# Performance work log

Hardware: AMD Instinct MI355X
Metric: run time of the kernel (lower is better)

Reference implementation:

```python
import jax, jax.numpy as jnp
import numpy as np

G, H, D = 8, 16, 64           # groups, heads-per-group, head_size
B, S = 2, 1024                # sequences, tokens per sequence (T = B*S packed)
HID = G * H * D               # 8192
SCALE = D ** -0.5


def _rotary(x, cos, sin):
    # NeoX-style rotary. x: [T, nh, D]; cos/sin: [T, D//2]
    half = D // 2
    c = cos[:, None, :]
    s = sin[:, None, :]
    x1, x2 = x[..., :half], x[..., half:]
    return jnp.concatenate([x1 * c - x2 * s, x2 * c + x1 * s], axis=-1)


def setup_inputs() -> dict:
    key = jax.random.key(0)
    ks = jax.random.split(key, 6)
    T = B * S
    hidden_states = jax.random.normal(ks[0], (T, HID), jnp.float32)
    # true rotary tables from positions (base 10000)
    pos = jnp.tile(jnp.arange(S, dtype=jnp.float32), B)            # [T]
    inv_freq = 1.0 / (10000.0 ** (jnp.arange(0, D, 2, dtype=jnp.float32) / D))
    freqs = pos[:, None] * inv_freq[None, :]                       # [T, D//2]
    cos, sin = jnp.cos(freqs), jnp.sin(freqs)
    w_qkv = jax.random.normal(ks[1], (HID, G * (H + 2) * D), jnp.float32) * (HID ** -0.5)
    b_qkv = jax.random.normal(ks[2], (G * (H + 2) * D,), jnp.float32) * 0.02
    w_dense = jax.random.normal(ks[3], (G * H * D, HID), jnp.float32) * (HID ** -0.5)
    b_dense = jax.random.normal(ks[4], (HID,), jnp.float32) * 0.02
    kv_cache = jnp.zeros((2, 4096, G, D), jnp.float32)
    slots = jnp.arange(T, dtype=jnp.int32)
    return dict(hidden_states=hidden_states, cos=cos, sin=sin,
                w_qkv=w_qkv, b_qkv=b_qkv, w_dense=w_dense, b_dense=b_dense,
                kv_cache=kv_cache, slots=slots, batch_size=B)


def reference(hidden_states, cos, sin, w_qkv, b_qkv, w_dense, b_dense,
              kv_cache, slots, batch_size):
    T = hidden_states.shape[0]
    qkv = hidden_states @ w_qkv + b_qkv                    # [T, G*(H+2)*D]
    qkv = qkv.reshape(T, G, H + 2, D)
    query = qkv[:, :, :H, :].reshape(T, G * H, D)          # [T, G*H, D]
    k = qkv[:, :, H, :]                                    # [T, G, D]
    v = qkv[:, :, H + 1, :]                                # [T, G, D]

    query = _rotary(query, cos, sin)
    k = _rotary(k, cos, sin)

    # reshape_and_cache: write rotated K and V into the slot cache
    new_cache = kv_cache.at[0, slots].set(k).at[1, slots].set(v)

    # prefill flash attention, causal, GQA (each group's K/V shared by H heads)
    q = query.reshape(batch_size, S, G, H, D)
    kb = k.reshape(batch_size, S, G, D)
    vb = v.reshape(batch_size, S, G, D)
    scores = jnp.einsum('bsghd,btgd->bghst', q, kb) * SCALE  # [B,G,H,S,S]
    causal = jnp.tril(jnp.ones((S, S), bool))
    scores = jnp.where(causal, scores, jnp.finfo(scores.dtype).min)
    probs = jax.nn.softmax(scores, axis=-1)
    attn = jnp.einsum('bghst,btgd->bsghd', probs, vb)        # [B,S,G,H,D]
    attn = attn.reshape(T, G * H * D)
    out = attn @ w_dense + b_dense                           # [T, HID]
    return out, new_cache
```

## Files before the change

kernel.cpp:

```cpp
#include <hip/hip_runtime.h>

#define T_TOK 2048
#define HIDD  8192
#define NQKV  9216
#define GG    8
#define HH    16
#define DD    64
#define SS    1024
#define BB    2
#define SCALE_ATTN 0.125f

typedef __attribute__((ext_vector_type(4))) float f32x4;
typedef __attribute__((ext_vector_type(8))) short bf16x8;

#define GLOBAL_AS __attribute__((address_space(1)))
#define LDS_AS    __attribute__((address_space(3)))

__device__ __forceinline__ void glds16(const void* g, void* l) {
  __builtin_amdgcn_global_load_lds((GLOBAL_AS void*)(g), (LDS_AS void*)(l), 16, 0, 0);
}

__device__ __forceinline__ ushort f2bf(float f) {
  union { float f; unsigned u; } v; v.f = f;
  unsigned u = v.u + 0x7fffu + ((v.u >> 16) & 1u);
  return (ushort)(u >> 16);
}

__global__ void cvt_bf16_kernel(const float* __restrict__ in, ushort* __restrict__ out, int n4) {
  int i = blockIdx.x * 256 + threadIdx.x;
  if (i >= n4) return;
  float4 v = ((const float4*)in)[i];
  ushort4 o;
  o.x = f2bf(v.x); o.y = f2bf(v.y); o.z = f2bf(v.z); o.w = f2bf(v.w);
  ((ushort4*)out)[i] = o;
}

__global__ void copy_f32_kernel(const float* __restrict__ in, float* __restrict__ out, int n4) {
  int i = blockIdx.x * 256 + threadIdx.x;
  if (i < n4) ((float4*)out)[i] = ((const float4*)in)[i];
}

__global__ __launch_bounds__(256) void transpose_bf16_kernel(
    const float* __restrict__ in, ushort* __restrict__ out, int R, int C)
{
  __shared__ float tile[64][65];
  const int c0 = blockIdx.x * 64, r0 = blockIdx.y * 64;
  const int tid = threadIdx.x;
  const int tx = tid & 15, iy = tid >> 4;
  #pragma unroll
  for (int p = 0; p < 4; ++p) {
    const int i = iy + p * 16;
    const float4 v = *(const float4*)&in[(size_t)(r0 + i) * C + c0 + tx * 4];
    tile[i][tx * 4 + 0] = v.x; tile[i][tx * 4 + 1] = v.y;
    tile[i][tx * 4 + 2] = v.z; tile[i][tx * 4 + 3] = v.w;
  }
  __syncthreads();
  const int r4 = tid & 15, cg = tid >> 4;
  #pragma unroll
  for (int p = 0; p < 4; ++p) {
    const int c = cg + p * 16;
    ushort4 o;
    o.x = f2bf(tile[r4 * 4 + 0][c]);
    o.y = f2bf(tile[r4 * 4 + 1][c]);
    o.z = f2bf(tile[r4 * 4 + 2][c]);
    o.w = f2bf(tile[r4 * 4 + 3][c]);
    *(ushort4*)&out[(size_t)(c0 + c) * R + r0 + r4 * 4] = o;
  }
}

__global__ __launch_bounds__(512, 2) void gemm_bt_kernel(
    const ushort* __restrict__ A, const ushort* __restrict__ Bt,
    const float* __restrict__ bias, float* __restrict__ C,
    int M, int N, int K)
{
  __shared__ __align__(16) ushort lds[4 * 16384];
  const int tid = threadIdx.x;
  const int wid = tid >> 6, lane = tid & 63;
  const int kg = lane >> 4, ln = lane & 15;

  const int nwg = gridDim.x * gridDim.y;
  const int lin = blockIdx.y * gridDim.x + blockIdx.x;
  const int swz = (lin & 7) * (nwg >> 3) + (lin >> 3);
  const int bx = swz % gridDim.x, by = swz / gridDim.x;

  const int m0 = by * 256, n0 = bx * 256;
  const int wm = (wid >> 2) << 7;
  const int wn = (wid & 3) << 6;

  f32x4 acc[8][4] = {};

  const int r0 = tid >> 2, sl = (tid & 3) * 8;
  const ushort* Ap0 = A  + (size_t)(m0 + r0) * K + sl;
  const ushort* Ap1 = A  + (size_t)(m0 + r0 + 128) * K + sl;
  const ushort* Bp0 = Bt + (size_t)(n0 + r0) * K + sl;
  const ushort* Bp1 = Bt + (size_t)(n0 + r0 + 128) * K + sl;
  ushort* wbA = lds + wid * 512;
  ushort* wbB = lds + 8192 + wid * 512;

  const int NT = K >> 5;

#define STAGE(t) {                                        \
    const int kk = (t) * 32;                              \
    const int bo = ((t) & 3) * 16384;                     \
    glds16(Ap0 + kk, wbA + bo);                           \
    glds16(Ap1 + kk, wbA + bo + 4096);                    \
    glds16(Bp0 + kk, wbB + bo);                           \
    glds16(Bp1 + kk, wbB + bo + 4096);                    \
  }

#define COMPUTE(t) {                                                          \
    const ushort* bufA = lds + ((t) & 3) * 16384;                             \
    const ushort* bufB = bufA + 8192;                                         \
    bf16x8 af[8], bv[4];                                                      \
    _Pragma("unroll")                                                         \
    for (int mi = 0; mi < 8; ++mi)                                            \
      af[mi] = *(const bf16x8*)&bufA[(wm + mi * 16 + ln) * 32 + kg * 8];      \
    _Pragma("unroll")                                                         \
    for (int ni = 0; ni < 4; ++ni)                                            \
      bv[ni] = *(const bf16x8*)&bufB[(wn + ni * 16 + ln) * 32 + kg * 8];      \
    __builtin_amdgcn_s_setprio(1);                                            \
    _Pragma("unroll")                                                         \
    for (int mi = 0; mi < 8; ++mi)                                            \
      _Pragma("unroll")                                                       \
      for (int ni = 0; ni < 4; ++ni)                                          \
        acc[mi][ni] = __builtin_amdgcn_mfma_f32_16x16x32_bf16(                \
            af[mi], bv[ni], acc[mi][ni], 0, 0, 0);                            \
    __builtin_amdgcn_s_setprio(0);                                            \
  }

  STAGE(0); STAGE(1); STAGE(2);

  for (int t = 0; t < NT - 3; ++t) {
    asm volatile("s_waitcnt vmcnt(8)" ::: "memory");
    __builtin_amdgcn_s_barrier();
    asm volatile("" ::: "memory");
    STAGE(t + 3);
    COMPUTE(t);
  }
  asm volatile("s_waitcnt vmcnt(8)" ::: "memory");
  __builtin_amdgcn_s_barrier();
  asm volatile("" ::: "memory");
  COMPUTE(NT - 3);
  asm volatile("s_waitcnt vmcnt(4)" ::: "memory");
  __builtin_amdgcn_s_barrier();
  asm volatile("" ::: "memory");
  COMPUTE(NT - 2);
  asm volatile("s_waitcnt vmcnt(0)" ::: "memory");
  __builtin_amdgcn_s_barrier();
  asm volatile("" ::: "memory");
  COMPUTE(NT - 1);

#undef STAGE
#undef COMPUTE

  #pragma unroll
  for (int mi = 0; mi < 8; ++mi) {
    const int row = m0 + wm + mi * 16 + kg * 4;
    #pragma unroll
    for (int ni = 0; ni < 4; ++ni) {
      const int col = n0 + wn + ni * 16 + ln;
      const float bvv = bias[col];
      #pragma unroll
      for (int r = 0; r < 4; ++r)
        C[(size_t)(row + r) * N + col] = acc[mi][ni][r] + bvv;
    }
  }
}

__global__ void rotary_scatter_kernel(const float* __restrict__ qkv,
                                      const float* __restrict__ cosb, const float* __restrict__ sinb,
                                      const int* __restrict__ slots,
                                      ushort* __restrict__ Qr, ushort* __restrict__ Kr,
                                      ushort* __restrict__ Vr, float* __restrict__ cache)
{
  const int t = blockIdx.x;
  const int b = t >> 10, s = t & 1023;
  const int slot = slots[t];
  for (int j = threadIdx.x; j < GG * 18 * 32; j += 256) {
    const int g = j / 576;
    const int rem = j - g * 576;
    const int head = rem >> 5;
    const int d = rem & 31;
    const float* row = qkv + (size_t)t * NQKV + g * 1152 + head * 64;
    const float x1 = row[d], x2 = row[d + 32];
    const float c = cosb[t * 32 + d], s_ = sinb[t * 32 + d];
    if (head < 16) {
      const size_t o = ((size_t)((b * 128 + g * 16 + head) * 1024 + s)) * 64;
      Qr[o + d]      = f2bf(x1 * c - x2 * s_);
      Qr[o + 32 + d] = f2bf(x2 * c + x1 * s_);
    } else if (head == 16) {
      const float o1 = x1 * c - x2 * s_, o2 = x2 * c + x1 * s_;
      const size_t o = ((size_t)((b * 8 + g) * 1024 + s)) * 64;
      Kr[o + d] = f2bf(o1); Kr[o + 32 + d] = f2bf(o2);
      const size_t co = ((size_t)slot * GG + g) * 64;
      cache[co + d] = o1; cache[co + 32 + d] = o2;
    } else {
      const size_t vo = ((size_t)((b * 8 + g) * 64 + d)) * 1024 + s;
      Vr[vo] = f2bf(x1);
      Vr[vo + (size_t)32 * 1024] = f2bf(x2);
      const size_t co = (size_t)4096 * GG * 64 + ((size_t)slot * GG + g) * 64;
      cache[co + d] = x1; cache[co + 32 + d] = x2;
    }
  }
}

__global__ __launch_bounds__(256, 4) void flash_attn_kernel(
    const ushort* __restrict__ Q, const ushort* __restrict__ Kc,
    const ushort* __restrict__ Vc, ushort* __restrict__ O)
{
  const int qb = blockIdx.x;
  const int gh = blockIdx.y;
  const int g  = gh >> 4;
  const int b  = blockIdx.z;
  const int tid = threadIdx.x;
  const int wid = tid >> 6, lane = tid & 63;
  const int kg = lane >> 4, ln = lane & 15;

  __shared__ __align__(16) ushort Ks[64 * 72];
  __shared__ __align__(16) ushort Vt[64 * 72];
  __shared__ __align__(16) ushort Ps[128 * 72];

  bf16x8 qf[2][2];
  #pragma unroll
  for (int st = 0; st < 2; ++st) {
    const int sq = qb * 128 + wid * 32 + st * 16 + ln;
    const size_t qoff = ((size_t)((b * 128 + gh) * 1024 + sq)) * 64;
    qf[st][0] = *(const bf16x8*)&Q[qoff + kg * 8];
    qf[st][1] = *(const bf16x8*)&Q[qoff + 32 + kg * 8];
  }

  f32x4 acc_o[2][4] = {};
  float m_i[2][4], l_i[2][4];
  #pragma unroll
  for (int st = 0; st < 2; ++st)
    #pragma unroll
    for (int r = 0; r < 4; ++r) { m_i[st][r] = -1e30f; l_i[st][r] = 0.f; }

  const size_t kbase = ((size_t)(b * 8 + g) * 1024) * 64;
  const size_t vbase = ((size_t)(b * 8 + g) * 64) * 1024;

  const int n_it = 2 * qb + 2;
  for (int it = 0; it < n_it; ++it) {
    const int t0 = it * 64;
    __syncthreads();
    #pragma unroll
    for (int rep = 0; rep < 2; ++rep) {
      const int idx = rep * 256 + tid;
      const int rr = idx >> 3, c8 = (idx & 7) * 8;
      *(uint4*)&Ks[rr * 72 + c8] = *(const uint4*)&Kc[kbase + (size_t)(t0 + rr) * 64 + c8];
      *(uint4*)&Vt[rr * 72 + c8] = *(const uint4*)&Vc[vbase + (size_t)rr * 1024 + t0 + c8];
    }
    __syncthreads();

    f32x4 sc[2][4];
    #pragma unroll
    for (int tt = 0; tt < 4; ++tt) {
      const bf16x8 kf0 = *(const bf16x8*)&Ks[(tt * 16 + ln) * 72 + kg * 8];
      const bf16x8 kf1 = *(const bf16x8*)&Ks[(tt * 16 + ln) * 72 + 32 + kg * 8];
      #pragma unroll
      for (int st = 0; st < 2; ++st) {
        f32x4 z = {};
        z = __builtin_amdgcn_mfma_f32_16x16x32_bf16(qf[st][0], kf0, z, 0, 0, 0);
        z = __builtin_amdgcn_mfma_f32_16x16x32_bf16(qf[st][1], kf1, z, 0, 0, 0);
        sc[st][tt] = z;
      }
    }

    if (it >= 2 * qb) {
      #pragma unroll
      for (int st = 0; st < 2; ++st) {
        const int srow = qb * 128 + wid * 32 + st * 16 + kg * 4;
        #pragma unroll
        for (int tt = 0; tt < 4; ++tt) {
          const int tg = t0 + tt * 16 + ln;
          #pragma unroll
          for (int r = 0; r < 4; ++r)
            sc[st][tt][r] = (tg <= srow + r) ? sc[st][tt][r] * SCALE_ATTN : -1e30f;
        }
      }
    } else {
      #pragma unroll
      for (int st = 0; st < 2; ++st)
        #pragma unroll
        for (int tt = 0; tt < 4; ++tt)
          #pragma unroll
          for (int r = 0; r < 4; ++r)
            sc[st][tt][r] *= SCALE_ATTN;
    }

    #pragma unroll
    for (int st = 0; st < 2; ++st) {
      float alpha[4];
      #pragma unroll
      for (int r = 0; r < 4; ++r) {
        float mx = fmaxf(fmaxf(sc[st][0][r], sc[st][1][r]), fmaxf(sc[st][2][r], sc[st][3][r]));
        #pragma unroll
        for (int off = 1; off < 16; off <<= 1)
          mx = fmaxf(mx, __shfl_xor(mx, off, 64));
        const float mn = fmaxf(m_i[st][r], mx);
        float rs = 0.f;
        #pragma unroll
        for (int tt = 0; tt < 4; ++tt) {
          const float p = __expf(sc[st][tt][r] - mn);
          sc[st][tt][r] = p; rs += p;
        }
        #pragma unroll
        for (int off = 1; off < 16; off <<= 1)
          rs += __shfl_xor(rs, off, 64);
        alpha[r] = __expf(m_i[st][r] - mn);
        l_i[st][r] = l_i[st][r] * alpha[r] + rs;
        m_i[st][r] = mn;
      }
      #pragma unroll
      for (int dt = 0; dt < 4; ++dt)
        #pragma unroll
        for (int r = 0; r < 4; ++r)
          acc_o[st][dt][r] *= alpha[r];
      #pragma unroll
      for (int tt = 0; tt < 4; ++tt)
        #pragma unroll
        for (int r = 0; r < 4; ++r)
          Ps[(wid * 32 + st * 16 + kg * 4 + r) * 72 + tt * 16 + ln] = f2bf(sc[st][tt][r]);
    }
    __syncthreads();

    #pragma unroll
    for (int c = 0; c < 2; ++c) {
      bf16x8 vf[4];
      #pragma unroll
      for (int dt = 0; dt < 4; ++dt)
        vf[dt] = *(const bf16x8*)&Vt[(dt * 16 + ln) * 72 + c * 32 + kg * 8];
      #pragma unroll
      for (int st = 0; st < 2; ++st) {
        const bf16x8 pf = *(const bf16x8*)&Ps[(wid * 32 + st * 16 + ln) * 72 + c * 32 + kg * 8];
        #pragma unroll
        for (int dt = 0; dt < 4; ++dt)
          acc_o[st][dt] = __builtin_amdgcn_mfma_f32_16x16x32_bf16(pf, vf[dt], acc_o[st][dt], 0, 0, 0);
      }
    }
  }

  #pragma unroll
  for (int st = 0; st < 2; ++st) {
    const int srow = qb * 128 + wid * 32 + st * 16 + kg * 4;
    #pragma unroll
    for (int dt = 0; dt < 4; ++dt) {
      #pragma unroll
      for (int r = 0; r < 4; ++r) {
        const float o = acc_o[st][dt][r] / l_i[st][r];
        O[((size_t)(b * 1024 + srow + r)) * 8192 + gh * 64 + dt * 16 + ln] = f2bf(o);
      }
    }
  }
}

#define WS0_HB   ((size_t)0)
#define WS1_WT   ((size_t)33554432)
#define WS2_QKV  ((size_t)(33554432 + 150994944))
#define WS3_QR   (WS2_QKV + (size_t)75497472)
#define WS4_KR   (WS3_QR + (size_t)33554432)
#define WS5_VR   (WS4_KR + (size_t)2097152)

extern "C" void kernel_launch(void* const* d_in, const int* in_sizes, int n_in,
                              void* d_out, int out_size, void* d_ws, size_t ws_size,
                              hipStream_t stream) {
  const float* hidden  = (const float*)d_in[0];
  const float* cosb    = (const float*)d_in[1];
  const float* sinb    = (const float*)d_in[2];
  const float* w_qkv   = (const float*)d_in[3];
  const float* b_qkv   = (const float*)d_in[4];
  const float* w_dense = (const float*)d_in[5];
  const float* b_dense = (const float*)d_in[6];
  const float* kv_in   = (const float*)d_in[7];
  const int*   slots   = (const int*)d_in[8];

  float* out = (float*)d_out;
  float* out_cache = out + (size_t)T_TOK * HIDD;

  char* ws = (char*)d_ws;
  ushort* hb   = (ushort*)(ws + WS0_HB);
  ushort* wT   = (ushort*)(ws + WS1_WT);
  float*  qkv  = (float*)(ws + WS2_QKV);
  ushort* qr   = (ushort*)(ws + WS3_QR);
  ushort* kr   = (ushort*)(ws + WS4_KR);
  ushort* vr   = (ushort*)(ws + WS5_VR);
  ushort* attn = hb;

  cvt_bf16_kernel<<<(T_TOK * HIDD / 4 + 255) / 256, 256, 0, stream>>>(hidden, hb, T_TOK * HIDD / 4);
  transpose_bf16_kernel<<<dim3(NQKV / 64, HIDD / 64), 256, 0, stream>>>(w_qkv, wT, HIDD, NQKV);
  gemm_bt_kernel<<<dim3(NQKV / 256, T_TOK / 256), 512, 0, stream>>>(hb, wT, b_qkv, qkv, T_TOK, NQKV, HIDD);
  copy_f32_kernel<<<(2 * 4096 * GG * DD / 4 + 255) / 256, 256, 0, stream>>>(kv_in, out_cache, 2 * 4096 * GG * DD / 4);
  rotary_scatter_kernel<<<T_TOK, 256, 0, stream>>>(qkv, cosb, sinb, slots, qr, kr, vr, out_cache);
  transpose_bf16_kernel<<<dim3(HIDD / 64, HIDD / 64), 256, 0, stream>>>(w_dense, wT, HIDD, HIDD);
  flash_attn_kernel<<<dim3(SS / 128, GG * HH, BB), 256, 0, stream>>>(qr, kr, vr, attn);
  gemm_bt_kernel<<<dim3(HIDD / 256, T_TOK / 256), 512, 0, stream>>>(attn, wT, b_dense, out, T_TOK, HIDD, HIDD);
}
```

Baseline: 1.794 ms.

## Restructure GEMM mainloop into 8-phase ping-pong schedule with swizzled K=64 LDS tiles

Replaces the 4-stage K=32 pipeline in the bf16 GEMM with a double-buffered K=64 scheme. Each K-tile's compute is split into four quarter-MFMA phases, each interleaved with a partial global-to-LDS stage and bracketed by barriers. It adds an XOR swizzle on LDS columns to avoid bank conflicts on the wider rows. The goal is finer overlap of global loads, LDS reads and MFMA work, at the cost of many more barriers and tighter vmcnt bookkeeping.

```diff
diff --git a/kernel.cpp b/kernel.cpp
--- a/kernel.cpp
+++ b/kernel.cpp
@@ -73,7 +73,7 @@
     const float* __restrict__ bias, float* __restrict__ C,
     int M, int N, int K)
 {
-  __shared__ __align__(16) ushort lds[4 * 16384];
+  __shared__ __align__(16) ushort lds[65536];
   const int tid = threadIdx.x;
   const int wid = tid >> 6, lane = tid & 63;
   const int kg = lane >> 4, ln = lane & 15;
@@ -86,72 +86,119 @@
   const int m0 = by * 256, n0 = bx * 256;
   const int wm = (wid >> 2) << 7;
   const int wn = (wid & 3) << 6;
+  const int hA = wm >> 7;
+  const int hB = wn >> 7;
+  const int brow0 = wn & 64;
 
   f32x4 acc[8][4] = {};
-
-  const int r0 = tid >> 2, sl = (tid & 3) * 8;
-  const ushort* Ap0 = A  + (size_t)(m0 + r0) * K + sl;
-  const ushort* Ap1 = A  + (size_t)(m0 + r0 + 128) * K + sl;
-  const ushort* Bp0 = Bt + (size_t)(n0 + r0) * K + sl;
-  const ushort* Bp1 = Bt + (size_t)(n0 + r0 + 128) * K + sl;
-  ushort* wbA = lds + wid * 512;
-  ushort* wbB = lds + 8192 + wid * 512;
-
-  const int NT = K >> 5;
-
-#define STAGE(t) {                                        \
-    const int kk = (t) * 32;                              \
-    const int bo = ((t) & 3) * 16384;                     \
-    glds16(Ap0 + kk, wbA + bo);                           \
-    glds16(Ap1 + kk, wbA + bo + 4096);                    \
-    glds16(Bp0 + kk, wbB + bo);                           \
-    glds16(Bp1 + kk, wbB + bo + 4096);                    \
-  }
-
-#define COMPUTE(t) {                                                          \
-    const ushort* bufA = lds + ((t) & 3) * 16384;                             \
-    const ushort* bufB = bufA + 8192;                                         \
-    bf16x8 af[8], bv[4];                                                      \
-    _Pragma("unroll")                                                         \
-    for (int mi = 0; mi < 8; ++mi)                                            \
-      af[mi] = *(const bf16x8*)&bufA[(wm + mi * 16 + ln) * 32 + kg * 8];      \
-    _Pragma("unroll")                                                         \
-    for (int ni = 0; ni < 4; ++ni)                                            \
-      bv[ni] = *(const bf16x8*)&bufB[(wn + ni * 16 + ln) * 32 + kg * 8];      \
-    __builtin_amdgcn_s_setprio(1);                                            \
-    _Pragma("unroll")                                                         \
-    for (int mi = 0; mi < 8; ++mi)                                            \
-      _Pragma("unroll")                                                       \
-      for (int ni = 0; ni < 4; ++ni)                                          \
-        acc[mi][ni] = __builtin_amdgcn_mfma_f32_16x16x32_bf16(                \
-            af[mi], bv[ni], acc[mi][ni], 0, 0, 0);                            \
-    __builtin_amdgcn_s_setprio(0);                                            \
-  }
-
-  STAGE(0); STAGE(1); STAGE(2);
-
-  for (int t = 0; t < NT - 3; ++t) {
-    asm volatile("s_waitcnt vmcnt(8)" ::: "memory");
-    __builtin_amdgcn_s_barrier();
-    asm volatile("" ::: "memory");
-    STAGE(t + 3);
-    COMPUTE(t);
-  }
-  asm volatile("s_waitcnt vmcnt(8)" ::: "memory");
-  __builtin_amdgcn_s_barrier();
-  asm volatile("" ::: "memory");
-  COMPUTE(NT - 3);
-  asm volatile("s_waitcnt vmcnt(4)" ::: "memory");
-  __builtin_amdgcn_s_barrier();
-  asm volatile("" ::: "memory");
-  COMPUTE(NT - 2);
-  asm volatile("s_waitcnt vmcnt(0)" ::: "memory");
-  __builtin_amdgcn_s_barrier();
-  asm volatile("" ::: "memory");
-  COMPUTE(NT - 1);
-
-#undef STAGE
-#undef COMPUTE
+  bf16x8 af[4][2], bv[4][2];
+
+  const int x0 = (kg    ) ^ (ln & 7);
+  const int x1 = (kg + 4) ^ (ln & 7);
+
+  const int r   = tid >> 3;
+  const int grp = (tid & 7) ^ (r & 7);
+  const ushort* Abase = A  + (size_t)(m0 + r) * K + grp * 8;
+  const ushort* Bbase = Bt + (size_t)(n0 + r) * K + grp * 8;
+  ushort* ldsw = lds + wid * 512;
+
+#define STG_A(kt, h) {                                                  \
+    const size_t go = (size_t)((h) * 128) * K + (size_t)(kt) * 64;      \
+    ushort* d_ = ldsw + (((kt) & 1) << 15) + ((h) << 13);               \
+    glds16(Abase + go, d_);                                             \
+    glds16(Abase + go + (size_t)64 * K, d_ + 4096); }
+#define STG_B(kt, h) {                                                  \
+    const size_t go = (size_t)((h) * 128) * K + (size_t)(kt) * 64;      \
+    ushort* d_ = ldsw + 16384 + (((kt) & 1) << 15) + ((h) << 13);       \
+    glds16(Bbase + go, d_);                                             \
+    glds16(Bbase + go + (size_t)64 * K, d_ + 4096); }
+
+#define LDA8(D, mi0) { _Pragma("unroll") for (int q = 0; q < 4; ++q) {  \
+    const int row_ = ((mi0) + q) * 16 + ln;                             \
+    const ushort* p_ = lds + ((D) << 15) + hA * 8192 + row_ * 64;       \
+    af[q][0] = *(const bf16x8*)&p_[x0 << 3];                            \
+    af[q][1] = *(const bf16x8*)&p_[x1 << 3]; } }
+#define LDB4(D, ni0) { _Pragma("unroll") for (int q = 0; q < 2; ++q) {  \
+    const int row_ = brow0 + ((ni0) + q) * 16 + ln;                     \
+    const ushort* p_ = lds + ((D) << 15) + 16384 + hB * 8192 + row_ * 64; \
+    bv[(ni0) + q][0] = *(const bf16x8*)&p_[x0 << 3];                    \
+    bv[(ni0) + q][1] = *(const bf16x8*)&p_[x1 << 3]; } }
+
+#define MMQ(mi0, ni0) { _Pragma("unroll") for (int q = 0; q < 4; ++q)   \
+    _Pragma("unroll") for (int n2 = 0; n2 < 2; ++n2) {                  \
+      acc[(mi0)+q][(ni0)+n2] = __builtin_amdgcn_mfma_f32_16x16x32_bf16( \
+          af[q][0], bv[(ni0)+n2][0], acc[(mi0)+q][(ni0)+n2], 0, 0, 0);  \
+      acc[(mi0)+q][(ni0)+n2] = __builtin_amdgcn_mfma_f32_16x16x32_bf16( \
+          af[q][1], bv[(ni0)+n2][1], acc[(mi0)+q][(ni0)+n2], 0, 0, 0); } }
+
+#define BAR   asm volatile("s_barrier" ::: "memory")
+#define LGKM  asm volatile("s_waitcnt lgkmcnt(0)" ::: "memory")
+#define VMC4  asm volatile("s_waitcnt vmcnt(4)" ::: "memory")
+#define VMC0  asm volatile("s_waitcnt vmcnt(0)" ::: "memory")
+#define PRIO1 __builtin_amdgcn_s_setprio(1)
+#define PRIO0 __builtin_amdgcn_s_setprio(0)
+
+  STG_A(0, 0); STG_A(0, 1); STG_B(0, 0); STG_B(0, 1);
+  STG_B(1, 0); STG_B(1, 1);
+  VMC4; BAR;
+
+  const int NI = K >> 7;
+  for (int i = 0; i < NI - 1; ++i) {
+    const int a = 2 * i, b = a + 1;
+    LDA8(0, 0); LDB4(0, 0);
+    STG_A(b, 0);
+    BAR; LGKM; PRIO1; MMQ(0, 0); PRIO0; BAR;
+    LDB4(0, 2);
+    STG_A(b, 1);
+    BAR; LGKM; PRIO1; MMQ(0, 2); PRIO0; BAR;
+    LDA8(0, 4);
+    STG_B(a + 2, 0);
+    BAR; LGKM; PRIO1; MMQ(4, 0); PRIO0; BAR;
+    STG_B(a + 2, 1);
+    BAR; LGKM; PRIO1; MMQ(4, 2); PRIO0; VMC4; BAR;
+    LDA8(1, 0); LDB4(1, 0);
+    STG_A(a + 2, 0);
+    BAR; LGKM; PRIO1; MMQ(0, 0); PRIO0; BAR;
+    LDB4(1, 2);
+    STG_A(a + 2, 1);
+    BAR; LGKM; PRIO1; MMQ(0, 2); PRIO0; BAR;
+    LDA8(1, 4);
+    STG_B(b + 2, 0);
+    BAR; LGKM; PRIO1; MMQ(4, 0); PRIO0; BAR;
+    STG_B(b + 2, 1);
+    BAR; LGKM; PRIO1; MMQ(4, 2); PRIO0; VMC4; BAR;
+  }
+  {
+    const int b = 2 * NI - 1;
+    LDA8(0, 0); LDB4(0, 0);
+    STG_A(b, 0);
+    BAR; LGKM; PRIO1; MMQ(0, 0); PRIO0; BAR;
+    LDB4(0, 2);
+    STG_A(b, 1);
+    BAR; LGKM; PRIO1; MMQ(0, 2); PRIO0; BAR;
+    LDA8(0, 4);
+    BAR; LGKM; PRIO1; MMQ(4, 0); PRIO0; BAR;
+    BAR; LGKM; PRIO1; MMQ(4, 2); PRIO0; VMC0; BAR;
+    LDA8(1, 0); LDB4(1, 0);
+    BAR; LGKM; PRIO1; MMQ(0, 0); PRIO0; BAR;
+    LDB4(1, 2);
+    BAR; LGKM; PRIO1; MMQ(0, 2); PRIO0; BAR;
+    LDA8(1, 4);
+    BAR; LGKM; PRIO1; MMQ(4, 0); PRIO0; BAR;
+    PRIO1; MMQ(4, 2); PRIO0;
+  }
+
+#undef STG_A
+#undef STG_B
+#undef LDA8
+#undef LDB4
+#undef MMQ
+#undef BAR
+#undef LGKM
+#undef VMC4
+#undef VMC0
+#undef PRIO1
+#undef PRIO0
 
   #pragma unroll
   for (int mi = 0; mi < 8; ++mi) {
@@ -161,8 +208,8 @@
       const int col = n0 + wn + ni * 16 + ln;
       const float bvv = bias[col];
       #pragma unroll
-      for (int r = 0; r < 4; ++r)
-        C[(size_t)(row + r) * N + col] = acc[mi][ni][r] + bvv;
+      for (int rr = 0; rr < 4; ++rr)
+        C[(size_t)(row + rr) * N + col] = acc[mi][ni][rr] + bvv;
     }
   }
 }
```

Result: faster. 1.646 ms (-8.2%).
